# Kernel tuning notes

Hardware: AMD Instinct MI355X
Metric: run time of the kernel (lower is better)

The kernel has to match this reference:

```python
import jax, jax.numpy as jnp
import numpy as np

EPS = 1e-8  # torch cosine_similarity eps


def setup_inputs() -> dict:
    key = jax.random.key(0)
    ks = jax.random.split(key, 8)
    B, D = 65536, 1024
    s = lambda fi, fo: (1.0 / np.sqrt(fi))
    return {
        "image_features": jax.random.normal(ks[0], (B, D), jnp.float32),
        "W1": jax.random.normal(ks[1], (D, 512), jnp.float32) * s(D, 512),
        "b1": jnp.zeros((512,), jnp.float32),
        "W2": jax.random.normal(ks[2], (512, 256), jnp.float32) * s(512, 256),
        "b2": jnp.zeros((256,), jnp.float32),
        "W3": jax.random.normal(ks[3], (256, 128), jnp.float32) * s(256, 128),
        "b3": jnp.zeros((128,), jnp.float32),
        "emb": jax.random.normal(ks[4], (1000, 128), jnp.float32),
    }


def reference(image_features, W1, b1, W2, b2, W3, b3, emb):
    # MLP projection (dropout is identity at inference)
    h = jax.nn.relu(image_features @ W1 + b1)
    h = jax.nn.relu(h @ W2 + b2)
    proj = h @ W3 + b3                              # [B, 128]
    # cosine similarity against all 1000 scene embeddings, fused as
    # normalize + small matmul instead of the broadcasted [B,1000,128] tensor
    pn = proj / jnp.maximum(jnp.linalg.norm(proj, axis=-1, keepdims=True), EPS)
    en = emb / jnp.maximum(jnp.linalg.norm(emb, axis=-1, keepdims=True), EPS)
    sims = pn @ en.T                                # [B, 1000]
    top_indices = jnp.argmax(sims, axis=1)          # [B]
    return top_indices
```

## Files before the change

kernel.cpp:

```cpp
#include <hip/hip_runtime.h>
#include <math.h>

#define EPS 1e-8f
#define TAU 1e-4f

typedef _Float16 half_t;
typedef __attribute__((ext_vector_type(8))) _Float16 f16x8;
typedef __attribute__((ext_vector_type(4))) float f32x4;

__device__ __forceinline__ void gload16(const half_t* g, half_t* l) {
    __builtin_amdgcn_global_load_lds((const __attribute__((address_space(1))) void*)g,
                                     (__attribute__((address_space(3))) void*)l, 16, 0, 0);
}

__device__ __forceinline__ void split2(float a, half_t& h, half_t& l) {
    h = (half_t)a;
    l = (half_t)(a - (float)h);
}


__global__ __launch_bounds__(64) void emb_norm_kernel(const float* __restrict__ emb,
                                                      float* __restrict__ enT) {
    const int row = blockIdx.x;
    const int t = threadIdx.x;
    float e0 = emb[row * 128 + t];
    float e1 = emb[row * 128 + 64 + t];
    float s = e0 * e0 + e1 * e1;
#pragma unroll
    for (int off = 32; off >= 1; off >>= 1) s += __shfl_xor(s, off);
    float denom = fmaxf(sqrtf(s), EPS);
    enT[(size_t)t * 1000 + row]        = e0 / denom;
    enT[(size_t)(64 + t) * 1000 + row] = e1 / denom;
}

__global__ __launch_bounds__(64) void emb_split_kernel(const float* __restrict__ emb,
                                                       half_t* __restrict__ eTh,
                                                       half_t* __restrict__ eTl) {
    const int n = blockIdx.x;
    const int t = threadIdx.x;
    float e0 = 0.f, e1 = 0.f;
    if (n < 1000) {
        e0 = emb[n * 128 + t];
        e1 = emb[n * 128 + 64 + t];
    }
    float s = e0 * e0 + e1 * e1;
#pragma unroll
    for (int off = 32; off >= 1; off >>= 1) s += __shfl_xor(s, off);
    float denom = fmaxf(sqrtf(s), EPS);
    float v0 = (n < 1000) ? e0 / denom : 0.f;
    float v1 = (n < 1000) ? e1 / denom : 0.f;
    half_t h, l;
    int f0 = t, f1 = 64 + t;
    size_t p0 = ((size_t)(f0 >> 3) * 1024 + n) * 8 + (f0 & 7);
    size_t p1 = ((size_t)(f1 >> 3) * 1024 + n) * 8 + (f1 & 7);
    split2(v0, h, l); eTh[p0] = h; eTl[p0] = l;
    split2(v1, h, l); eTh[p1] = h; eTl[p1] = l;
}

template<int N>
__global__ __launch_bounds__(256) void wsplit_kernel(const float* __restrict__ W,
                                                     half_t* __restrict__ Wh,
                                                     half_t* __restrict__ Wl) {
    int idx = blockIdx.x * 256 + threadIdx.x;
    int k = idx / N, n = idx % N;
    float w = W[idx];
    half_t h, l;
    split2(w, h, l);
    size_t pos = ((size_t)(k >> 3) * N + n) * 8 + (k & 7);
    Wh[pos] = h; Wl[pos] = l;
}

#define EPI_RELU 0
#define EPI_NORM 1
#define EPI_TOP2 2

template<int K, int N, bool AF32, int EPI>
__global__ __launch_bounds__(256, 2) void gemm16(
    const float* __restrict__ A32,
    const half_t* __restrict__ Agh, const half_t* __restrict__ Agl,
    const half_t* __restrict__ Bgh, const half_t* __restrict__ Bgl,
    const float* __restrict__ bias,
    half_t* __restrict__ Oh, half_t* __restrict__ Ol,
    float* __restrict__ pv1, int* __restrict__ pi1, float* __restrict__ pv2,
    int Mtot)
{
    __shared__ alignas(16) half_t sAh[8][128][8];
    __shared__ alignas(16) half_t sAl[8][128][8];
    __shared__ alignas(16) half_t sBh[8][128][8];
    __shared__ alignas(16) half_t sBl[8][128][8];

    const int t = threadIdx.x;
    const int lane = t & 63, w = t >> 6;
    const int lr = lane & 15, lg = lane >> 4;
    const int wm = w >> 1, wn = w & 1;

    const int nwg = gridDim.x * gridDim.y;
    const int lin = blockIdx.x + gridDim.x * blockIdx.y;
    const int cpx = nwg >> 3;
    const int logical = (lin & 7) * cpx + (lin >> 3);
    const int bx = logical % gridDim.x;
    const int by = logical / gridDim.x;
    const int m0 = by * 128, n0 = bx * 128;

    f32x4 acc[4][4] = {};

    for (int k0 = 0; k0 < K; k0 += 64) {
        if constexpr (AF32) {
#pragma unroll
            for (int q = 0; q < 4; ++q) {
                int s = t + 256 * q;
                int row = s >> 3, kb = s & 7;
                const float* src = A32 + (size_t)(m0 + row) * K + k0 + kb * 8;
                float4 v0 = *(const float4*)src;
                float4 v1 = *(const float4*)(src + 4);
                float vv[8] = {v0.x, v0.y, v0.z, v0.w, v1.x, v1.y, v1.z, v1.w};
                f16x8 hi, lo;
#pragma unroll
                for (int i = 0; i < 8; ++i) {
                    half_t h = (half_t)vv[i];
                    hi[i] = h;
                    lo[i] = (half_t)(vv[i] - (float)h);
                }
                int prow = row ^ kb;
                *(f16x8*)&sAh[kb][prow][0] = hi;
                *(f16x8*)&sAl[kb][prow][0] = lo;
            }
        } else {
#pragma unroll
            for (int i = 0; i < 4; ++i) {
                int s = (w << 8) + (i << 6) + lane;
                int kb = s >> 7, prow = s & 127;
                int row = prow ^ kb;
                size_t go = (size_t)(m0 + row) * K + k0 + kb * 8;
                gload16(Agh + go, &sAh[0][0][0] + (size_t)s * 8);
                gload16(Agl + go, &sAl[0][0][0] + (size_t)s * 8);
            }
        }
#pragma unroll
        for (int i = 0; i < 4; ++i) {
            int s = (w << 8) + (i << 6) + lane;
            int kb = s >> 7, col = s & 127;
            size_t go = ((size_t)(k0 / 8 + kb) * N + n0 + col) * 8;
            gload16(Bgh + go, &sBh[0][0][0] + (size_t)s * 8);
            gload16(Bgl + go, &sBl[0][0][0] + (size_t)s * 8);
        }
        __syncthreads();
#pragma unroll
        for (int ks = 0; ks < 2; ++ks) {
            const int kb = ks * 4 + lg;
            f16x8 ah[4], al[4], bh[4], bl[4];
#pragma unroll
            for (int mf = 0; mf < 4; ++mf) {
                int row = wm * 64 + mf * 16 + lr;
                int prow = row ^ kb;
                ah[mf] = *(const f16x8*)&sAh[kb][prow][0];
                al[mf] = *(const f16x8*)&sAl[kb][prow][0];
            }
#pragma unroll
            for (int nf = 0; nf < 4; ++nf) {
                int col = wn * 64 + nf * 16 + lr;
                bh[nf] = *(const f16x8*)&sBh[kb][col][0];
                bl[nf] = *(const f16x8*)&sBl[kb][col][0];
            }
#pragma unroll
            for (int mf = 0; mf < 4; ++mf)
#pragma unroll
                for (int nf = 0; nf < 4; ++nf) {
                    acc[mf][nf] = __builtin_amdgcn_mfma_f32_16x16x32_f16(ah[mf], bh[nf], acc[mf][nf], 0, 0, 0);
                    acc[mf][nf] = __builtin_amdgcn_mfma_f32_16x16x32_f16(ah[mf], bl[nf], acc[mf][nf], 0, 0, 0);
                    acc[mf][nf] = __builtin_amdgcn_mfma_f32_16x16x32_f16(al[mf], bh[nf], acc[mf][nf], 0, 0, 0);
                }
        }
        __syncthreads();
    }

    if constexpr (EPI == EPI_RELU) {
#pragma unroll
        for (int nf = 0; nf < 4; ++nf) {
            int n = n0 + wn * 64 + nf * 16 + lr;
            float bb = bias[n];
#pragma unroll
            for (int mf = 0; mf < 4; ++mf)
#pragma unroll
                for (int r = 0; r < 4; ++r) {
                    int m = m0 + wm * 64 + mf * 16 + lg * 4 + r;
                    float v = acc[mf][nf][r] + bb;
                    v = fmaxf(v, 0.f);
                    half_t h, l;
                    split2(v, h, l);
                    Oh[(size_t)m * N + n] = h;
                    Ol[(size_t)m * N + n] = l;
                }
        }
    } else if constexpr (EPI == EPI_NORM) {
        __shared__ float nsum[2][128];
#pragma unroll
        for (int nf = 0; nf < 4; ++nf) {
            float bb = bias[wn * 64 + nf * 16 + lr];
#pragma unroll
            for (int mf = 0; mf < 4; ++mf)
#pragma unroll
                for (int r = 0; r < 4; ++r) acc[mf][nf][r] += bb;
        }
#pragma unroll
        for (int mf = 0; mf < 4; ++mf)
#pragma unroll
            for (int r = 0; r < 4; ++r) {
                float s = 0.f;
#pragma unroll
                for (int nf = 0; nf < 4; ++nf) {
                    float v = acc[mf][nf][r];
                    s += v * v;
                }
#pragma unroll
                for (int off = 1; off < 16; off <<= 1) s += __shfl_xor(s, off);
                if (lr == 0) nsum[wn][wm * 64 + mf * 16 + lg * 4 + r] = s;
            }
        __syncthreads();
#pragma unroll
        for (int mf = 0; mf < 4; ++mf)
#pragma unroll
            for (int r = 0; r < 4; ++r) {
                int ml = wm * 64 + mf * 16 + lg * 4 + r;
                float tot = nsum[0][ml] + nsum[1][ml];
                float sc = 1.0f / fmaxf(sqrtf(tot), EPS);
                int m = m0 + ml;
#pragma unroll
                for (int nf = 0; nf < 4; ++nf) {
                    int n = wn * 64 + nf * 16 + lr;
                    float v = acc[mf][nf][r] * sc;
                    half_t h, l;
                    split2(v, h, l);
                    Oh[(size_t)m * 128 + n] = h;
                    Ol[(size_t)m * 128 + n] = l;
                }
            }
    } else {
        __shared__ float sv1[2][128];
        __shared__ int   si1[2][128];
        __shared__ float sv2[2][128];
#pragma unroll
        for (int mf = 0; mf < 4; ++mf)
#pragma unroll
            for (int r = 0; r < 4; ++r) {
                float v1 = -INFINITY, v2 = -INFINITY;
                int i1 = 0;
#pragma unroll
                for (int nf = 0; nf < 4; ++nf) {
                    int n = n0 + wn * 64 + nf * 16 + lr;
                    float v = (n < 1000) ? acc[mf][nf][r] : -INFINITY;
                    if (v > v1) { v2 = v1; v1 = v; i1 = n; }
                    else if (v > v2) v2 = v;
                }
#pragma unroll
                for (int off = 1; off < 16; off <<= 1) {
                    float ov1 = __shfl_xor(v1, off);
                    int   oi1 = __shfl_xor(i1, off);
                    float ov2 = __shfl_xor(v2, off);
                    if (ov1 > v1) { v2 = fmaxf(v1, ov2); v1 = ov1; i1 = oi1; }
                    else if (ov1 == v1) { v2 = fmaxf(v2, ov1); if (oi1 < i1) i1 = oi1; }
                    else { v2 = fmaxf(v2, ov1); }
                }
                if (lr == 0) {
                    int ml = wm * 64 + mf * 16 + lg * 4 + r;
                    sv1[wn][ml] = v1; si1[wn][ml] = i1; sv2[wn][ml] = v2;
                }
            }
        __syncthreads();
        if (t < 128) {
            float v1 = sv1[0][t]; int i1 = si1[0][t]; float v2 = sv2[0][t];
            float ov1 = sv1[1][t]; int oi1 = si1[1][t]; float ov2 = sv2[1][t];
            if (ov1 > v1) { v2 = fmaxf(v1, ov2); v1 = ov1; i1 = oi1; }
            else if (ov1 == v1) { v2 = fmaxf(v2, ov1); if (oi1 < i1) i1 = oi1; }
            else { v2 = fmaxf(v2, ov1); }
            size_t p = (size_t)bx * Mtot + m0 + t;
            pv1[p] = v1; pi1[p] = i1; pv2[p] = v2;
        }
    }
}

__global__ __launch_bounds__(256) void finalize_kernel(
    const float* __restrict__ pv1, const int* __restrict__ pi1, const float* __restrict__ pv2,
    int* __restrict__ out, int* __restrict__ list, int* __restrict__ count, int Mtot)
{
    int r = blockIdx.x * 256 + threadIdx.x;
    float v1 = -INFINITY, v2 = -INFINITY;
    int i1 = 0;
#pragma unroll
    for (int nb = 0; nb < 8; ++nb) {
        size_t p = (size_t)nb * Mtot + r;
        float ov1 = pv1[p]; int oi1 = pi1[p]; float ov2 = pv2[p];
        if (ov1 > v1) { v2 = fmaxf(v1, ov2); v1 = ov1; i1 = oi1; }
        else if (ov1 == v1) { v2 = fmaxf(v2, ov1); if (oi1 < i1) i1 = oi1; }
        else { v2 = fmaxf(v2, ov1); }
    }
    out[r] = i1;
    if (v1 - v2 < TAU) {
        int p = atomicAdd(count, 1);
        if (p < Mtot) list[p] = r;
    }
}

__global__ void zero_count_kernel(int* c) { if (threadIdx.x == 0) *c = 0; }

__global__ __launch_bounds__(256) void recheck_row_kernel(
    const float* __restrict__ img,
    const float* __restrict__ W1, const float* __restrict__ b1,
    const float* __restrict__ W2, const float* __restrict__ b2,
    const float* __restrict__ W3, const float* __restrict__ b3,
    const float* __restrict__ enT,
    const int* __restrict__ list, const int* __restrict__ count,
    int* __restrict__ out, int maxcnt)
{
    __shared__ float sx[1024];
    __shared__ float sh1[512];
    __shared__ float sh2[256];
    __shared__ float sp[128];
    __shared__ float sden;
    __shared__ float redv[4];
    __shared__ int   redi[4];

    const int t = threadIdx.x;
    const int lane = t & 63, wv = t >> 6;
    int cnt = *count;
    if (cnt > maxcnt) cnt = maxcnt;

    for (int b = blockIdx.x; b < cnt; b += gridDim.x) {
        const int row = list[b];
        *(float4*)&sx[t * 4] = *(const float4*)(img + (size_t)row * 1024 + t * 4);
        __syncthreads();
        {
            float a0 = 0.f, a1 = 0.f;
#pragma unroll 8
            for (int k = 0; k < 1024; ++k) {
                float xv = sx[k];
                float2 wv2 = *(const float2*)(W1 + (size_t)k * 512 + 2 * t);
                a0 = fmaf(xv, wv2.x, a0);
                a1 = fmaf(xv, wv2.y, a1);
            }
            sh1[2 * t]     = fmaxf(a0 + b1[2 * t], 0.f);
            sh1[2 * t + 1] = fmaxf(a1 + b1[2 * t + 1], 0.f);
        }
        __syncthreads();
        {
            float a = 0.f;
#pragma unroll 8
            for (int k = 0; k < 512; ++k)
                a = fmaf(sh1[k], W2[(size_t)k * 256 + t], a);
            sh2[t] = fmaxf(a + b2[t], 0.f);
        }
        __syncthreads();
        if (t < 128) {
            float a = 0.f;
#pragma unroll 8
            for (int k = 0; k < 256; ++k)
                a = fmaf(sh2[k], W3[(size_t)k * 128 + t], a);
            sp[t] = a + b3[t];
        }
        __syncthreads();
        if (t < 64) {
            float s = sp[t] * sp[t] + sp[t + 64] * sp[t + 64];
#pragma unroll
            for (int off = 32; off >= 1; off >>= 1) s += __shfl_xor(s, off);
            if (t == 0) sden = fmaxf(sqrtf(s), EPS);
        }
        __syncthreads();
        if (t < 128) sp[t] = sp[t] / sden;
        __syncthreads();
        float bm = -INFINITY;
        int bi = 0;
#pragma unroll
        for (int j = 0; j < 4; ++j) {
            const int c = t + 256 * j;
            if (c < 1000) {
                float a = 0.f;
#pragma unroll 8
                for (int k = 0; k < 128; ++k)
                    a = fmaf(sp[k], enT[(size_t)k * 1000 + c], a);
                if (a > bm) { bm = a; bi = c; }
            }
        }
#pragma unroll
        for (int off = 1; off < 64; off <<= 1) {
            float om = __shfl_xor(bm, off);
            int oi = __shfl_xor(bi, off);
            if (om > bm || (om == bm && oi < bi)) { bm = om; bi = oi; }
        }
        if (lane == 0) { redv[wv] = bm; redi[wv] = bi; }
        __syncthreads();
        if (t == 0) {
            float v = redv[0]; int i = redi[0];
#pragma unroll
            for (int q = 1; q < 4; ++q) {
                if (redv[q] > v || (redv[q] == v && redi[q] < i)) { v = redv[q]; i = redi[q]; }
            }
            out[row] = i;
        }
        __syncthreads();
    }
}

__global__ __launch_bounds__(256) void scene_exact_kernel(
    const float* __restrict__ img,
    const float* __restrict__ W1, const float* __restrict__ b1,
    const float* __restrict__ W2, const float* __restrict__ b2,
    const float* __restrict__ W3, const float* __restrict__ b3,
    const float* __restrict__ enT,
    int* __restrict__ out)
{
    __shared__ float sImg[16][64];
    __shared__ float sH1[16][512];
    __shared__ float sH2[16][256];
    __shared__ float sPn[16][128];

    const int tid = threadIdx.x;
    const int base = blockIdx.x * 16;

    {
        const int tx = tid & 63, ty = tid >> 6;
        float acc[4][8] = {};
        for (int k0 = 0; k0 < 1024; k0 += 64) {
            {
                const int r = tid >> 4, c4 = tid & 15;
                float4 v = *(const float4*)(img + (size_t)(base + r) * 1024 + k0 + c4 * 4);
                *(float4*)(&sImg[r][c4 * 4]) = v;
            }
            __syncthreads();
#pragma unroll 4
            for (int kk = 0; kk < 64; ++kk) {
                const int k = k0 + kk;
                float a[4];
#pragma unroll
                for (int i = 0; i < 4; ++i) a[i] = sImg[ty + 4 * i][kk];
#pragma unroll
                for (int j = 0; j < 8; ++j) {
                    float wv = W1[(size_t)k * 512 + tx + 64 * j];
#pragma unroll
                    for (int i = 0; i < 4; ++i) acc[i][j] = fmaf(a[i], wv, acc[i][j]);
                }
            }
            __syncthreads();
        }
#pragma unroll
        for (int j = 0; j < 8; ++j) {
            float bb = b1[tx + 64 * j];
#pragma unroll
            for (int i = 0; i < 4; ++i) {
                float v = acc[i][j] + bb;
                sH1[ty + 4 * i][tx + 64 * j] = v > 0.f ? v : 0.f;
            }
        }
        __syncthreads();
    }
    {
        const int tx = tid & 63, ty = tid >> 6;
        float acc[4][4] = {};
#pragma unroll 4
        for (int k = 0; k < 512; ++k) {
            float a[4];
#pragma unroll
            for (int i = 0; i < 4; ++i) a[i] = sH1[ty + 4 * i][k];
#pragma unroll
            for (int j = 0; j < 4; ++j) {
                float wv = W2[(size_t)k * 256 + tx + 64 * j];
#pragma unroll
                for (int i = 0; i < 4; ++i) acc[i][j] = fmaf(a[i], wv, acc[i][j]);
            }
        }
        __syncthreads();
#pragma unroll
        for (int j = 0; j < 4; ++j) {
            float bb = b2[tx + 64 * j];
#pragma unroll
            for (int i = 0; i < 4; ++i) {
                float v = acc[i][j] + bb;
                sH2[ty + 4 * i][tx + 64 * j] = v > 0.f ? v : 0.f;
            }
        }
        __syncthreads();
    }
    {
        const int tx = tid & 31, ty = tid >> 5;
        float acc[2][4] = {};
#pragma unroll 4
        for (int k = 0; k < 256; ++k) {
            float a[2];
#pragma unroll
            for (int i = 0; i < 2; ++i) a[i] = sH2[ty + 8 * i][k];
#pragma unroll
            for (int j = 0; j < 4; ++j) {
                float wv = W3[(size_t)k * 128 + tx + 32 * j];
#pragma unroll
                for (int i = 0; i < 2; ++i) acc[i][j] = fmaf(a[i], wv, acc[i][j]);
            }
        }
#pragma unroll
        for (int j = 0; j < 4; ++j) {
            float bb = b3[tx + 32 * j];
#pragma unroll
            for (int i = 0; i < 2; ++i) sPn[ty + 8 * i][tx + 32 * j] = acc[i][j] + bb;
        }
        __syncthreads();
    }
    {
        const int r = tid >> 4, sub = tid & 15;
        float s = 0.f;
#pragma unroll
        for (int m = 0; m < 8; ++m) {
            float v = sPn[r][sub + 16 * m];
            s += v * v;
        }
#pragma unroll
        for (int off = 1; off < 16; off <<= 1) s += __shfl_xor(s, off);
        float denom = fmaxf(sqrtf(s), EPS);
#pragma unroll
        for (int m = 0; m < 8; ++m) sPn[r][sub + 16 * m] /= denom;
        __syncthreads();
    }
    {
        const int ct = tid & 63, rg = tid >> 6;
        float bm[4]; int bi[4];
#pragma unroll
        for (int i = 0; i < 4; ++i) { bm[i] = -INFINITY; bi[i] = 0; }
#pragma unroll
        for (int tpass = 0; tpass < 2; ++tpass) {
            const int tt = ct + 64 * tpass;
            if (tt < 125) {
                const int c0 = tt * 8;
                float acc[4][8] = {};
#pragma unroll 4
                for (int k = 0; k < 128; ++k) {
                    float p[4];
#pragma unroll
                    for (int i = 0; i < 4; ++i) p[i] = sPn[rg * 4 + i][k];
                    const float* ep = enT + (size_t)k * 1000 + c0;
                    float4 e0 = *(const float4*)(ep);
                    float4 e1 = *(const float4*)(ep + 4);
                    float e[8] = {e0.x, e0.y, e0.z, e0.w, e1.x, e1.y, e1.z, e1.w};
#pragma unroll
                    for (int j = 0; j < 8; ++j)
#pragma unroll
                        for (int i = 0; i < 4; ++i) acc[i][j] = fmaf(p[i], e[j], acc[i][j]);
                }
#pragma unroll
                for (int j = 0; j < 8; ++j) {
                    const int c = c0 + j;
#pragma unroll
                    for (int i = 0; i < 4; ++i)
                        if (acc[i][j] > bm[i]) { bm[i] = acc[i][j]; bi[i] = c; }
                }
            }
        }
#pragma unroll
        for (int off = 1; off < 64; off <<= 1) {
#pragma unroll
            for (int i = 0; i < 4; ++i) {
                float om = __shfl_xor(bm[i], off);
                int oi = __shfl_xor(bi[i], off);
                if (om > bm[i] || (om == bm[i] && oi < bi[i])) { bm[i] = om; bi[i] = oi; }
            }
        }
        if (ct == 0) {
#pragma unroll
            for (int i = 0; i < 4; ++i) out[base + rg * 4 + i] = bi[i];
        }
    }
}

extern "C" void kernel_launch(void* const* d_in, const int* in_sizes, int n_in,
                              void* d_out, int out_size, void* d_ws, size_t ws_size,
                              hipStream_t stream) {
    const float* img = (const float*)d_in[0];
    const float* W1  = (const float*)d_in[1];
    const float* b1  = (const float*)d_in[2];
    const float* W2  = (const float*)d_in[3];
    const float* b2  = (const float*)d_in[4];
    const float* W3  = (const float*)d_in[5];
    const float* b3  = (const float*)d_in[6];
    const float* emb = (const float*)d_in[7];
    int* out = (int*)d_out;
    const int B = in_sizes[0] / 1024;

    size_t off = 0;
    auto carve = [&](size_t bytes) {
        void* p = (char*)d_ws + off;
        off += (bytes + 255) & ~(size_t)255;
        return p;
    };
    float*  enT  = (float*)carve(128 * 1000 * 4);
    half_t* W1h  = (half_t*)carve((size_t)1024 * 512 * 2);
    half_t* W1l  = (half_t*)carve((size_t)1024 * 512 * 2);
    half_t* W2h  = (half_t*)carve((size_t)512 * 256 * 2);
    half_t* W2l  = (half_t*)carve((size_t)512 * 256 * 2);
    half_t* W3h  = (half_t*)carve((size_t)256 * 128 * 2);
    half_t* W3l  = (half_t*)carve((size_t)256 * 128 * 2);
    half_t* eTh  = (half_t*)carve((size_t)16 * 1024 * 8 * 2);
    half_t* eTl  = (half_t*)carve((size_t)16 * 1024 * 8 * 2);
    half_t* h1h  = (half_t*)carve((size_t)B * 512 * 2);
    half_t* h1l  = (half_t*)carve((size_t)B * 512 * 2);
    half_t* h2h  = (half_t*)carve((size_t)B * 256 * 2);
    half_t* h2l  = (half_t*)carve((size_t)B * 256 * 2);
    const size_t REQUIRE = off;

    if (ws_size < REQUIRE) {
        emb_norm_kernel<<<1000, 64, 0, stream>>>(emb, (float*)d_ws);
        scene_exact_kernel<<<B / 16, 256, 0, stream>>>(
            img, W1, b1, W2, b2, W3, b3, (float*)d_ws, out);
        return;
    }

    half_t* pnh  = h1h;
    half_t* pnl  = (half_t*)((char*)h1h + (size_t)B * 128 * 2);
    float*  pv1  = (float*)((char*)h1h + (size_t)B * 128 * 4);
    int*    pi1  = (int*)((char*)pv1 + (size_t)8 * B * 4);
    float*  pv2  = (float*)((char*)pi1 + (size_t)8 * B * 4);
    int*    list = (int*)((char*)pv2 + (size_t)8 * B * 4);
    int*    cnt  = (int*)((char*)list + (size_t)B * 4);

    emb_norm_kernel<<<1000, 64, 0, stream>>>(emb, enT);
    emb_split_kernel<<<1024, 64, 0, stream>>>(emb, eTh, eTl);
    wsplit_kernel<512><<<(1024 * 512) / 256, 256, 0, stream>>>(W1, W1h, W1l);
    wsplit_kernel<256><<<(512 * 256) / 256, 256, 0, stream>>>(W2, W2h, W2l);
    wsplit_kernel<128><<<(256 * 128) / 256, 256, 0, stream>>>(W3, W3h, W3l);

    gemm16<1024, 512, true, EPI_RELU><<<dim3(4, B / 128), 256, 0, stream>>>(
        img, nullptr, nullptr, W1h, W1l, b1, h1h, h1l, nullptr, nullptr, nullptr, B);
    gemm16<512, 256, false, EPI_RELU><<<dim3(2, B / 128), 256, 0, stream>>>(
        nullptr, h1h, h1l, W2h, W2l, b2, h2h, h2l, nullptr, nullptr, nullptr, B);
    gemm16<256, 128, false, EPI_NORM><<<dim3(1, B / 128), 256, 0, stream>>>(
        nullptr, h2h, h2l, W3h, W3l, b3, pnh, pnl, nullptr, nullptr, nullptr, B);
    gemm16<128, 1024, false, EPI_TOP2><<<dim3(8, B / 128), 256, 0, stream>>>(
        nullptr, pnh, pnl, eTh, eTl, nullptr, nullptr, nullptr, pv1, pi1, pv2, B);

    zero_count_kernel<<<1, 64, 0, stream>>>(cnt);
    finalize_kernel<<<B / 256, 256, 0, stream>>>(pv1, pi1, pv2, out, list, cnt, B);
    recheck_row_kernel<<<2048, 256, 0, stream>>>(
        img, W1, b1, W2, b2, W3, b3, enT, list, cnt, out, B);
}
```

Baseline: 621.9 us.

## Fuse third GEMM, normalization, similarity GEMM and top-2 into one kernel

Replaces the separate layer-3 GEMM with norm epilogue, the similarity GEMM with per-tile top-2 partials, and the finalize kernel with one proj_sims kernel. Each 128-row block computes the projection, normalizes it into LDS, loops over the eight 128-column embedding tiles while keeping a running top-2 in registers, and writes the argmax and recheck list directly. This drops the global round trips for the normalized projection and the partial top-2 arrays, plus two launches. In exchange it uses 128 KB of LDS per block with one block per CU, and the embedding tiles are loaded without double buffering.

```diff
diff --git a/kernel.cpp b/kernel.cpp
--- a/kernel.cpp
+++ b/kernel.cpp
@@ -70,19 +70,13 @@
     Wh[pos] = h; Wl[pos] = l;
 }
 
-#define EPI_RELU 0
-#define EPI_NORM 1
-#define EPI_TOP2 2
-
-template<int K, int N, bool AF32, int EPI>
+template<int K, int N, bool AF32>
 __global__ __launch_bounds__(256, 2) void gemm16(
     const float* __restrict__ A32,
     const half_t* __restrict__ Agh, const half_t* __restrict__ Agl,
     const half_t* __restrict__ Bgh, const half_t* __restrict__ Bgl,
     const float* __restrict__ bias,
-    half_t* __restrict__ Oh, half_t* __restrict__ Ol,
-    float* __restrict__ pv1, int* __restrict__ pi1, float* __restrict__ pv2,
-    int Mtot)
+    half_t* __restrict__ Oh, half_t* __restrict__ Ol)
 {
     __shared__ alignas(16) half_t sAh[8][128][8];
     __shared__ alignas(16) half_t sAl[8][128][8];
@@ -174,134 +168,234 @@
         __syncthreads();
     }
 
-    if constexpr (EPI == EPI_RELU) {
-#pragma unroll
-        for (int nf = 0; nf < 4; ++nf) {
-            int n = n0 + wn * 64 + nf * 16 + lr;
-            float bb = bias[n];
+#pragma unroll
+    for (int nf = 0; nf < 4; ++nf) {
+        int n = n0 + wn * 64 + nf * 16 + lr;
+        float bb = bias[n];
+#pragma unroll
+        for (int mf = 0; mf < 4; ++mf)
+#pragma unroll
+            for (int r = 0; r < 4; ++r) {
+                int m = m0 + wm * 64 + mf * 16 + lg * 4 + r;
+                float v = acc[mf][nf][r] + bb;
+                v = fmaxf(v, 0.f);
+                half_t h, l;
+                split2(v, h, l);
+                Oh[(size_t)m * N + n] = h;
+                Ol[(size_t)m * N + n] = l;
+            }
+    }
+}
+
+__global__ void zero_count_kernel(int* c) { if (threadIdx.x == 0) *c = 0; }
+
+__global__ __launch_bounds__(256, 1) void proj_sims_kernel(
+    const half_t* __restrict__ h2h, const half_t* __restrict__ h2l,
+    const half_t* __restrict__ W3h, const half_t* __restrict__ W3l,
+    const float* __restrict__ b3,
+    const half_t* __restrict__ eTh, const half_t* __restrict__ eTl,
+    int* __restrict__ out, int* __restrict__ list, int* __restrict__ cnt,
+    int Mtot)
+{
+    __shared__ alignas(16) unsigned char smem[131072];
+    half_t* sAh = (half_t*)smem;
+    half_t* sAl = sAh + 8 * 128 * 8;
+    half_t* sBh = sAl + 8 * 128 * 8;
+    half_t* sBl = sBh + 8 * 128 * 8;
+    half_t* sPnH = (half_t*)(smem + 65536);
+    half_t* sPnL = sPnH + 16 * 128 * 8;
+    half_t* eH = (half_t*)smem;
+    half_t* eL = eH + 16 * 128 * 8;
+    float* nsum = (float*)smem;
+    float* sv1 = (float*)smem;
+    int*   si1 = (int*)(smem + 1024);
+    float* sv2 = (float*)(smem + 2048);
+
+    const int t = threadIdx.x;
+    const int lane = t & 63, w = t >> 6;
+    const int lr = lane & 15, lg = lane >> 4;
+    const int wm = w >> 1, wn = w & 1;
+    const int m0 = blockIdx.x * 128;
+
+    f32x4 acc[4][4] = {};
+    for (int k0 = 0; k0 < 256; k0 += 64) {
+#pragma unroll
+        for (int i = 0; i < 4; ++i) {
+            int s = (w << 8) + (i << 6) + lane;
+            int kb = s >> 7, prow = s & 127;
+            int row = prow ^ kb;
+            size_t go = (size_t)(m0 + row) * 256 + k0 + kb * 8;
+            gload16(h2h + go, sAh + (size_t)s * 8);
+            gload16(h2l + go, sAl + (size_t)s * 8);
+            int col = s & 127;
+            size_t gb = ((size_t)(k0 / 8 + kb) * 128 + col) * 8;
+            gload16(W3h + gb, sBh + (size_t)s * 8);
+            gload16(W3l + gb, sBl + (size_t)s * 8);
+        }
+        __syncthreads();
+#pragma unroll
+        for (int ks = 0; ks < 2; ++ks) {
+            const int kb = ks * 4 + lg;
+            f16x8 ah[4], al[4], bh[4], bl[4];
+#pragma unroll
+            for (int mf = 0; mf < 4; ++mf) {
+                int prow = (wm * 64 + mf * 16 + lr) ^ kb;
+                ah[mf] = *(const f16x8*)(sAh + ((size_t)kb * 128 + prow) * 8);
+                al[mf] = *(const f16x8*)(sAl + ((size_t)kb * 128 + prow) * 8);
+            }
+#pragma unroll
+            for (int nf = 0; nf < 4; ++nf) {
+                int col = wn * 64 + nf * 16 + lr;
+                bh[nf] = *(const f16x8*)(sBh + ((size_t)kb * 128 + col) * 8);
+                bl[nf] = *(const f16x8*)(sBl + ((size_t)kb * 128 + col) * 8);
+            }
 #pragma unroll
             for (int mf = 0; mf < 4; ++mf)
 #pragma unroll
+                for (int nf = 0; nf < 4; ++nf) {
+                    acc[mf][nf] = __builtin_amdgcn_mfma_f32_16x16x32_f16(ah[mf], bh[nf], acc[mf][nf], 0, 0, 0);
+                    acc[mf][nf] = __builtin_amdgcn_mfma_f32_16x16x32_f16(ah[mf], bl[nf], acc[mf][nf], 0, 0, 0);
+                    acc[mf][nf] = __builtin_amdgcn_mfma_f32_16x16x32_f16(al[mf], bh[nf], acc[mf][nf], 0, 0, 0);
+                }
+        }
+        __syncthreads();
+    }
+
+#pragma unroll
+    for (int nf = 0; nf < 4; ++nf) {
+        float bb = b3[wn * 64 + nf * 16 + lr];
+#pragma unroll
+        for (int mf = 0; mf < 4; ++mf)
+#pragma unroll
+            for (int r = 0; r < 4; ++r) acc[mf][nf][r] += bb;
+    }
+#pragma unroll
+    for (int mf = 0; mf < 4; ++mf)
+#pragma unroll
+        for (int r = 0; r < 4; ++r) {
+            float s = 0.f;
+#pragma unroll
+            for (int nf = 0; nf < 4; ++nf) {
+                float v = acc[mf][nf][r];
+                s += v * v;
+            }
+#pragma unroll
+            for (int off = 1; off < 16; off <<= 1) s += __shfl_xor(s, off);
+            if (lr == 0) nsum[wn * 128 + wm * 64 + mf * 16 + lg * 4 + r] = s;
+        }
+    __syncthreads();
+#pragma unroll
+    for (int mf = 0; mf < 4; ++mf)
+#pragma unroll
+        for (int r = 0; r < 4; ++r) {
+            int row = wm * 64 + mf * 16 + lg * 4 + r;
+            float tot = nsum[row] + nsum[128 + row];
+            float sc = 1.0f / fmaxf(sqrtf(tot), EPS);
+#pragma unroll
+            for (int nf = 0; nf < 4; ++nf) {
+                int col = wn * 64 + nf * 16 + lr;
+                int kb = col >> 3, i = col & 7;
+                int prow = row ^ kb;
+                half_t h, l;
+                split2(acc[mf][nf][r] * sc, h, l);
+                sPnH[((size_t)kb * 128 + prow) * 8 + i] = h;
+                sPnL[((size_t)kb * 128 + prow) * 8 + i] = l;
+            }
+        }
+    __syncthreads();
+
+    float tv1[4][4], tv2[4][4];
+    int ti1[4][4];
+#pragma unroll
+    for (int mf = 0; mf < 4; ++mf)
+#pragma unroll
+        for (int r = 0; r < 4; ++r) { tv1[mf][r] = -INFINITY; tv2[mf][r] = -INFINITY; ti1[mf][r] = 0; }
+
+    for (int nt = 0; nt < 8; ++nt) {
+#pragma unroll
+        for (int i = 0; i < 8; ++i) {
+            int s = t + 256 * i;
+            int kb = s >> 7, col = s & 127;
+            size_t go = ((size_t)kb * 1024 + nt * 128 + col) * 8;
+            gload16(eTh + go, eH + (size_t)s * 8);
+            gload16(eTl + go, eL + (size_t)s * 8);
+        }
+        __syncthreads();
+        f32x4 acc2[4][4] = {};
+#pragma unroll
+        for (int ks = 0; ks < 4; ++ks) {
+            const int kb = ks * 4 + lg;
+            f16x8 ah[4], al[4], bh[4], bl[4];
+#pragma unroll
+            for (int mf = 0; mf < 4; ++mf) {
+                int prow = (wm * 64 + mf * 16 + lr) ^ kb;
+                ah[mf] = *(const f16x8*)(sPnH + ((size_t)kb * 128 + prow) * 8);
+                al[mf] = *(const f16x8*)(sPnL + ((size_t)kb * 128 + prow) * 8);
+            }
+#pragma unroll
+            for (int nf = 0; nf < 4; ++nf) {
+                int col = wn * 64 + nf * 16 + lr;
+                bh[nf] = *(const f16x8*)(eH + ((size_t)kb * 128 + col) * 8);
+                bl[nf] = *(const f16x8*)(eL + ((size_t)kb * 128 + col) * 8);
+            }
+#pragma unroll
+            for (int mf = 0; mf < 4; ++mf)
+#pragma unroll
+                for (int nf = 0; nf < 4; ++nf) {
+                    acc2[mf][nf] = __builtin_amdgcn_mfma_f32_16x16x32_f16(ah[mf], bh[nf], acc2[mf][nf], 0, 0, 0);
+                    acc2[mf][nf] = __builtin_amdgcn_mfma_f32_16x16x32_f16(ah[mf], bl[nf], acc2[mf][nf], 0, 0, 0);
+                    acc2[mf][nf] = __builtin_amdgcn_mfma_f32_16x16x32_f16(al[mf], bh[nf], acc2[mf][nf], 0, 0, 0);
+                }
+        }
+#pragma unroll
+        for (int mf = 0; mf < 4; ++mf)
+#pragma unroll
+            for (int nf = 0; nf < 4; ++nf) {
+                int gc = nt * 128 + wn * 64 + nf * 16 + lr;
+#pragma unroll
                 for (int r = 0; r < 4; ++r) {
-                    int m = m0 + wm * 64 + mf * 16 + lg * 4 + r;
-                    float v = acc[mf][nf][r] + bb;
-                    v = fmaxf(v, 0.f);
-                    half_t h, l;
-                    split2(v, h, l);
-                    Oh[(size_t)m * N + n] = h;
-                    Ol[(size_t)m * N + n] = l;
+                    float v = (gc < 1000) ? acc2[mf][nf][r] : -INFINITY;
+                    if (v > tv1[mf][r]) { tv2[mf][r] = tv1[mf][r]; tv1[mf][r] = v; ti1[mf][r] = gc; }
+                    else if (v > tv2[mf][r]) tv2[mf][r] = v;
                 }
-        }
-    } else if constexpr (EPI == EPI_NORM) {
-        __shared__ float nsum[2][128];
-#pragma unroll
-        for (int nf = 0; nf < 4; ++nf) {
-            float bb = bias[wn * 64 + nf * 16 + lr];
-#pragma unroll
-            for (int mf = 0; mf < 4; ++mf)
-#pragma unroll
-                for (int r = 0; r < 4; ++r) acc[mf][nf][r] += bb;
-        }
-#pragma unroll
-        for (int mf = 0; mf < 4; ++mf)
-#pragma unroll
-            for (int r = 0; r < 4; ++r) {
-                float s = 0.f;
-#pragma unroll
-                for (int nf = 0; nf < 4; ++nf) {
-                    float v = acc[mf][nf][r];
-                    s += v * v;
-                }
-#pragma unroll
-                for (int off = 1; off < 16; off <<= 1) s += __shfl_xor(s, off);
-                if (lr == 0) nsum[wn][wm * 64 + mf * 16 + lg * 4 + r] = s;
-            }
-        __syncthreads();
-#pragma unroll
-        for (int mf = 0; mf < 4; ++mf)
-#pragma unroll
-            for (int r = 0; r < 4; ++r) {
+            }
+        __syncthreads();
+    }
+
+#pragma unroll
+    for (int mf = 0; mf < 4; ++mf)
+#pragma unroll
+        for (int r = 0; r < 4; ++r) {
+            float v1 = tv1[mf][r], v2 = tv2[mf][r];
+            int i1 = ti1[mf][r];
+#pragma unroll
+            for (int off = 1; off < 16; off <<= 1) {
+                float ov1 = __shfl_xor(v1, off);
+                int   oi1 = __shfl_xor(i1, off);
+                float ov2 = __shfl_xor(v2, off);
+                if (ov1 > v1) { v2 = fmaxf(v1, ov2); v1 = ov1; i1 = oi1; }
+                else if (ov1 == v1) { v2 = fmaxf(v2, ov1); if (oi1 < i1) i1 = oi1; }
+                else { v2 = fmaxf(v2, ov1); }
+            }
+            if (lr == 0) {
                 int ml = wm * 64 + mf * 16 + lg * 4 + r;
-                float tot = nsum[0][ml] + nsum[1][ml];
-                float sc = 1.0f / fmaxf(sqrtf(tot), EPS);
-                int m = m0 + ml;
-#pragma unroll
-                for (int nf = 0; nf < 4; ++nf) {
-                    int n = wn * 64 + nf * 16 + lr;
-                    float v = acc[mf][nf][r] * sc;
-                    half_t h, l;
-                    split2(v, h, l);
-                    Oh[(size_t)m * 128 + n] = h;
-                    Ol[(size_t)m * 128 + n] = l;
-                }
-            }
-    } else {
-        __shared__ float sv1[2][128];
-        __shared__ int   si1[2][128];
-        __shared__ float sv2[2][128];
-#pragma unroll
-        for (int mf = 0; mf < 4; ++mf)
-#pragma unroll
-            for (int r = 0; r < 4; ++r) {
-                float v1 = -INFINITY, v2 = -INFINITY;
-                int i1 = 0;
-#pragma unroll
-                for (int nf = 0; nf < 4; ++nf) {
-                    int n = n0 + wn * 64 + nf * 16 + lr;
-                    float v = (n < 1000) ? acc[mf][nf][r] : -INFINITY;
-                    if (v > v1) { v2 = v1; v1 = v; i1 = n; }
-                    else if (v > v2) v2 = v;
-                }
-#pragma unroll
-                for (int off = 1; off < 16; off <<= 1) {
-                    float ov1 = __shfl_xor(v1, off);
-                    int   oi1 = __shfl_xor(i1, off);
-                    float ov2 = __shfl_xor(v2, off);
-                    if (ov1 > v1) { v2 = fmaxf(v1, ov2); v1 = ov1; i1 = oi1; }
-                    else if (ov1 == v1) { v2 = fmaxf(v2, ov1); if (oi1 < i1) i1 = oi1; }
-                    else { v2 = fmaxf(v2, ov1); }
-                }
-                if (lr == 0) {
-                    int ml = wm * 64 + mf * 16 + lg * 4 + r;
-                    sv1[wn][ml] = v1; si1[wn][ml] = i1; sv2[wn][ml] = v2;
-                }
-            }
-        __syncthreads();
-        if (t < 128) {
-            float v1 = sv1[0][t]; int i1 = si1[0][t]; float v2 = sv2[0][t];
-            float ov1 = sv1[1][t]; int oi1 = si1[1][t]; float ov2 = sv2[1][t];
-            if (ov1 > v1) { v2 = fmaxf(v1, ov2); v1 = ov1; i1 = oi1; }
-            else if (ov1 == v1) { v2 = fmaxf(v2, ov1); if (oi1 < i1) i1 = oi1; }
-            else { v2 = fmaxf(v2, ov1); }
-            size_t p = (size_t)bx * Mtot + m0 + t;
-            pv1[p] = v1; pi1[p] = i1; pv2[p] = v2;
-        }
-    }
-}
-
-__global__ __launch_bounds__(256) void finalize_kernel(
-    const float* __restrict__ pv1, const int* __restrict__ pi1, const float* __restrict__ pv2,
-    int* __restrict__ out, int* __restrict__ list, int* __restrict__ count, int Mtot)
-{
-    int r = blockIdx.x * 256 + threadIdx.x;
-    float v1 = -INFINITY, v2 = -INFINITY;
-    int i1 = 0;
-#pragma unroll
-    for (int nb = 0; nb < 8; ++nb) {
-        size_t p = (size_t)nb * Mtot + r;
-        float ov1 = pv1[p]; int oi1 = pi1[p]; float ov2 = pv2[p];
+                sv1[wn * 128 + ml] = v1; si1[wn * 128 + ml] = i1; sv2[wn * 128 + ml] = v2;
+            }
+        }
+    __syncthreads();
+    if (t < 128) {
+        float v1 = sv1[t]; int i1 = si1[t]; float v2 = sv2[t];
+        float ov1 = sv1[128 + t]; int oi1 = si1[128 + t]; float ov2 = sv2[128 + t];
         if (ov1 > v1) { v2 = fmaxf(v1, ov2); v1 = ov1; i1 = oi1; }
         else if (ov1 == v1) { v2 = fmaxf(v2, ov1); if (oi1 < i1) i1 = oi1; }
         else { v2 = fmaxf(v2, ov1); }
-    }
-    out[r] = i1;
-    if (v1 - v2 < TAU) {
-        int p = atomicAdd(count, 1);
-        if (p < Mtot) list[p] = r;
-    }
-}
-
-__global__ void zero_count_kernel(int* c) { if (threadIdx.x == 0) *c = 0; }
+        out[m0 + t] = i1;
+        if (v1 - v2 < TAU) {
+            int p = atomicAdd(cnt, 1);
+            if (p < Mtot) list[p] = m0 + t;
+        }
+    }
+}
 
 __global__ __launch_bounds__(256) void recheck_row_kernel(
     const float* __restrict__ img,
@@ -609,13 +703,8 @@
         return;
     }
 
-    half_t* pnh  = h1h;
-    half_t* pnl  = (half_t*)((char*)h1h + (size_t)B * 128 * 2);
-    float*  pv1  = (float*)((char*)h1h + (size_t)B * 128 * 4);
-    int*    pi1  = (int*)((char*)pv1 + (size_t)8 * B * 4);
-    float*  pv2  = (float*)((char*)pi1 + (size_t)8 * B * 4);
-    int*    list = (int*)((char*)pv2 + (size_t)8 * B * 4);
-    int*    cnt  = (int*)((char*)list + (size_t)B * 4);
+    int* list = (int*)h1h;
+    int* cnt  = (int*)((char*)h1h + (size_t)B * 4);
 
     emb_norm_kernel<<<1000, 64, 0, stream>>>(emb, enT);
     emb_split_kernel<<<1024, 64, 0, stream>>>(emb, eTh, eTl);
@@ -623,17 +712,15 @@
     wsplit_kernel<256><<<(512 * 256) / 256, 256, 0, stream>>>(W2, W2h, W2l);
     wsplit_kernel<128><<<(256 * 128) / 256, 256, 0, stream>>>(W3, W3h, W3l);
 
-    gemm16<1024, 512, true, EPI_RELU><<<dim3(4, B / 128), 256, 0, stream>>>(
-        img, nullptr, nullptr, W1h, W1l, b1, h1h, h1l, nullptr, nullptr, nullptr, B);
-    gemm16<512, 256, false, EPI_RELU><<<dim3(2, B / 128), 256, 0, stream>>>(
-        nullptr, h1h, h1l, W2h, W2l, b2, h2h, h2l, nullptr, nullptr, nullptr, B);
-    gemm16<256, 128, false, EPI_NORM><<<dim3(1, B / 128), 256, 0, stream>>>(
-        nullptr, h2h, h2l, W3h, W3l, b3, pnh, pnl, nullptr, nullptr, nullptr, B);
-    gemm16<128, 1024, false, EPI_TOP2><<<dim3(8, B / 128), 256, 0, stream>>>(
-        nullptr, pnh, pnl, eTh, eTl, nullptr, nullptr, nullptr, pv1, pi1, pv2, B);
+    gemm16<1024, 512, true><<<dim3(4, B / 128), 256, 0, stream>>>(
+        img, nullptr, nullptr, W1h, W1l, b1, h1h, h1l);
+    gemm16<512, 256, false><<<dim3(2, B / 128), 256, 0, stream>>>(
+        nullptr, h1h, h1l, W2h, W2l, b2, h2h, h2l);
 
     zero_count_kernel<<<1, 64, 0, stream>>>(cnt);
-    finalize_kernel<<<B / 256, 256, 0, stream>>>(pv1, pi1, pv2, out, list, cnt, B);
+    proj_sims_kernel<<<B / 128, 256, 0, stream>>>(
+        h2h, h2l, W3h, W3l, b3, eTh, eTl, out, list, cnt, B);
+
     recheck_row_kernel<<<2048, 256, 0, stream>>>(
         img, W1, b1, W2, b2, W3, b3, enT, list, cnt, out, B);
 }
```

Result: slower. 1.133 ms (+82.2%).

## Fuse similarity GEMM, top-2 reduction and finalize into one row-tiled kernel

Applied to the files above, without the earlier changes.

Replaces the 128x128-tiled similarity GEMM with per-N-tile partial top-2 outputs plus a separate finalize kernel by a single kernel. Each block keeps a 64-row slice of normalized projections resident in LDS and streams all 16 embedding column tiles, holding a running top-2 in registers. The block then writes the argmax and ambiguous-row list directly. This removes the partial-result buffers, their global round trip and one launch. In exchange, embedding tiles are reloaded per 64-row block and loads are not double-buffered, so each tile waits on its load.

```diff
diff --git a/kernel.cpp b/kernel.cpp
--- a/kernel.cpp
+++ b/kernel.cpp
@@ -72,7 +72,6 @@
 
 #define EPI_RELU 0
 #define EPI_NORM 1
-#define EPI_TOP2 2
 
 template<int K, int N, bool AF32, int EPI>
 __global__ __launch_bounds__(256, 2) void gemm16(
@@ -80,9 +79,7 @@
     const half_t* __restrict__ Agh, const half_t* __restrict__ Agl,
     const half_t* __restrict__ Bgh, const half_t* __restrict__ Bgl,
     const float* __restrict__ bias,
-    half_t* __restrict__ Oh, half_t* __restrict__ Ol,
-    float* __restrict__ pv1, int* __restrict__ pi1, float* __restrict__ pv2,
-    int Mtot)
+    half_t* __restrict__ Oh, half_t* __restrict__ Ol)
 {
     __shared__ alignas(16) half_t sAh[8][128][8];
     __shared__ alignas(16) half_t sAl[8][128][8];
@@ -192,7 +189,7 @@
                     Ol[(size_t)m * N + n] = l;
                 }
         }
-    } else if constexpr (EPI == EPI_NORM) {
+    } else {
         __shared__ float nsum[2][128];
 #pragma unroll
         for (int nf = 0; nf < 4; ++nf) {
@@ -235,73 +232,143 @@
                     Ol[(size_t)m * 128 + n] = l;
                 }
             }
-    } else {
-        __shared__ float sv1[2][128];
-        __shared__ int   si1[2][128];
-        __shared__ float sv2[2][128];
-#pragma unroll
-        for (int mf = 0; mf < 4; ++mf)
-#pragma unroll
-            for (int r = 0; r < 4; ++r) {
-                float v1 = -INFINITY, v2 = -INFINITY;
-                int i1 = 0;
-#pragma unroll
-                for (int nf = 0; nf < 4; ++nf) {
-                    int n = n0 + wn * 64 + nf * 16 + lr;
-                    float v = (n < 1000) ? acc[mf][nf][r] : -INFINITY;
-                    if (v > v1) { v2 = v1; v1 = v; i1 = n; }
-                    else if (v > v2) v2 = v;
-                }
-#pragma unroll
-                for (int off = 1; off < 16; off <<= 1) {
-                    float ov1 = __shfl_xor(v1, off);
-                    int   oi1 = __shfl_xor(i1, off);
-                    float ov2 = __shfl_xor(v2, off);
-                    if (ov1 > v1) { v2 = fmaxf(v1, ov2); v1 = ov1; i1 = oi1; }
-                    else if (ov1 == v1) { v2 = fmaxf(v2, ov1); if (oi1 < i1) i1 = oi1; }
-                    else { v2 = fmaxf(v2, ov1); }
-                }
-                if (lr == 0) {
-                    int ml = wm * 64 + mf * 16 + lg * 4 + r;
-                    sv1[wn][ml] = v1; si1[wn][ml] = i1; sv2[wn][ml] = v2;
-                }
-            }
-        __syncthreads();
-        if (t < 128) {
-            float v1 = sv1[0][t]; int i1 = si1[0][t]; float v2 = sv2[0][t];
-            float ov1 = sv1[1][t]; int oi1 = si1[1][t]; float ov2 = sv2[1][t];
-            if (ov1 > v1) { v2 = fmaxf(v1, ov2); v1 = ov1; i1 = oi1; }
-            else if (ov1 == v1) { v2 = fmaxf(v2, ov1); if (oi1 < i1) i1 = oi1; }
-            else { v2 = fmaxf(v2, ov1); }
-            size_t p = (size_t)bx * Mtot + m0 + t;
-            pv1[p] = v1; pi1[p] = i1; pv2[p] = v2;
-        }
-    }
-}
-
-__global__ __launch_bounds__(256) void finalize_kernel(
-    const float* __restrict__ pv1, const int* __restrict__ pi1, const float* __restrict__ pv2,
-    int* __restrict__ out, int* __restrict__ list, int* __restrict__ count, int Mtot)
+    }
+}
+
+__global__ void zero_count_kernel(int* c) { if (threadIdx.x == 0) *c = 0; }
+
+__global__ __launch_bounds__(256, 2) void sims64_kernel(
+    const half_t* __restrict__ pnh, const half_t* __restrict__ pnl,
+    const half_t* __restrict__ eTh, const half_t* __restrict__ eTl,
+    int* __restrict__ out, int* __restrict__ list, int* __restrict__ cnt,
+    int Mtot)
 {
-    int r = blockIdx.x * 256 + threadIdx.x;
-    float v1 = -INFINITY, v2 = -INFINITY;
-    int i1 = 0;
-#pragma unroll
-    for (int nb = 0; nb < 8; ++nb) {
-        size_t p = (size_t)nb * Mtot + r;
-        float ov1 = pv1[p]; int oi1 = pi1[p]; float ov2 = pv2[p];
+    __shared__ alignas(16) half_t sPnH[16 * 64 * 8];
+    __shared__ alignas(16) half_t sPnL[16 * 64 * 8];
+    __shared__ alignas(16) half_t sEH[16 * 64 * 8];
+    __shared__ alignas(16) half_t sEL[16 * 64 * 8];
+    __shared__ float sv1[128];
+    __shared__ int   si1[128];
+    __shared__ float sv2[128];
+
+    const int t = threadIdx.x;
+    const int lane = t & 63, w = t >> 6;
+    const int lr = lane & 15, lg = lane >> 4;
+    const int wm = w >> 1, wn = w & 1;
+    const int m0 = blockIdx.x * 64;
+
+#pragma unroll
+    for (int i = 0; i < 4; ++i) {
+        int s = t + 256 * i;
+        int kb = s >> 6, row = s & 63;
+        size_t go = (size_t)(m0 + row) * 128 + kb * 8;
+        gload16(pnh + go, sPnH + (size_t)s * 8);
+        gload16(pnl + go, sPnL + (size_t)s * 8);
+    }
+#pragma unroll
+    for (int i = 0; i < 4; ++i) {
+        int s = t + 256 * i;
+        int kb = s >> 6, col = s & 63;
+        size_t go = ((size_t)kb * 1024 + col) * 8;
+        gload16(eTh + go, sEH + (size_t)s * 8);
+        gload16(eTl + go, sEL + (size_t)s * 8);
+    }
+
+    float tv1[2][4], tv2[2][4];
+    int ti1[2][4];
+#pragma unroll
+    for (int mf = 0; mf < 2; ++mf)
+#pragma unroll
+        for (int r = 0; r < 4; ++r) { tv1[mf][r] = -INFINITY; tv2[mf][r] = -INFINITY; ti1[mf][r] = 0; }
+
+    for (int nt = 0; nt < 16; ++nt) {
+        __syncthreads();
+        f32x4 acc[2][2] = {};
+#pragma unroll
+        for (int ks = 0; ks < 4; ++ks) {
+            const int kb = ks * 4 + lg;
+            f16x8 ah[2], al[2], bh[2], bl[2];
+#pragma unroll
+            for (int mf = 0; mf < 2; ++mf) {
+                int row = wm * 32 + mf * 16 + lr;
+                ah[mf] = *(const f16x8*)(sPnH + ((size_t)kb * 64 + row) * 8);
+                al[mf] = *(const f16x8*)(sPnL + ((size_t)kb * 64 + row) * 8);
+            }
+#pragma unroll
+            for (int nf = 0; nf < 2; ++nf) {
+                int col = wn * 32 + nf * 16 + lr;
+                bh[nf] = *(const f16x8*)(sEH + ((size_t)kb * 64 + col) * 8);
+                bl[nf] = *(const f16x8*)(sEL + ((size_t)kb * 64 + col) * 8);
+            }
+#pragma unroll
+            for (int mf = 0; mf < 2; ++mf)
+#pragma unroll
+                for (int nf = 0; nf < 2; ++nf) {
+                    acc[mf][nf] = __builtin_amdgcn_mfma_f32_16x16x32_f16(ah[mf], bh[nf], acc[mf][nf], 0, 0, 0);
+                    acc[mf][nf] = __builtin_amdgcn_mfma_f32_16x16x32_f16(ah[mf], bl[nf], acc[mf][nf], 0, 0, 0);
+                    acc[mf][nf] = __builtin_amdgcn_mfma_f32_16x16x32_f16(al[mf], bh[nf], acc[mf][nf], 0, 0, 0);
+                }
+        }
+#pragma unroll
+        for (int mf = 0; mf < 2; ++mf)
+#pragma unroll
+            for (int nf = 0; nf < 2; ++nf) {
+                int gc = nt * 64 + wn * 32 + nf * 16 + lr;
+#pragma unroll
+                for (int r = 0; r < 4; ++r) {
+                    float v = (gc < 1000) ? acc[mf][nf][r] : -INFINITY;
+                    if (v > tv1[mf][r]) { tv2[mf][r] = tv1[mf][r]; tv1[mf][r] = v; ti1[mf][r] = gc; }
+                    else if (v > tv2[mf][r]) tv2[mf][r] = v;
+                }
+            }
+        __syncthreads();
+        if (nt < 15) {
+            int ntn = nt + 1;
+#pragma unroll
+            for (int i = 0; i < 4; ++i) {
+                int s = t + 256 * i;
+                int kb = s >> 6, col = s & 63;
+                size_t go = ((size_t)kb * 1024 + ntn * 64 + col) * 8;
+                gload16(eTh + go, sEH + (size_t)s * 8);
+                gload16(eTl + go, sEL + (size_t)s * 8);
+            }
+        }
+    }
+
+#pragma unroll
+    for (int mf = 0; mf < 2; ++mf)
+#pragma unroll
+        for (int r = 0; r < 4; ++r) {
+            float v1 = tv1[mf][r], v2 = tv2[mf][r];
+            int i1 = ti1[mf][r];
+#pragma unroll
+            for (int off = 1; off < 16; off <<= 1) {
+                float ov1 = __shfl_xor(v1, off);
+                int   oi1 = __shfl_xor(i1, off);
+                float ov2 = __shfl_xor(v2, off);
+                if (ov1 > v1) { v2 = fmaxf(v1, ov2); v1 = ov1; i1 = oi1; }
+                else if (ov1 == v1) { v2 = fmaxf(v2, ov1); if (oi1 < i1) i1 = oi1; }
+                else { v2 = fmaxf(v2, ov1); }
+            }
+            if (lr == 0) {
+                int ml = wm * 32 + mf * 16 + lg * 4 + r;
+                sv1[wn * 64 + ml] = v1; si1[wn * 64 + ml] = i1; sv2[wn * 64 + ml] = v2;
+            }
+        }
+    __syncthreads();
+    if (t < 64) {
+        float v1 = sv1[t]; int i1 = si1[t]; float v2 = sv2[t];
+        float ov1 = sv1[64 + t]; int oi1 = si1[64 + t]; float ov2 = sv2[64 + t];
         if (ov1 > v1) { v2 = fmaxf(v1, ov2); v1 = ov1; i1 = oi1; }
         else if (ov1 == v1) { v2 = fmaxf(v2, ov1); if (oi1 < i1) i1 = oi1; }
         else { v2 = fmaxf(v2, ov1); }
-    }
-    out[r] = i1;
-    if (v1 - v2 < TAU) {
-        int p = atomicAdd(count, 1);
-        if (p < Mtot) list[p] = r;
-    }
-}
-
-__global__ void zero_count_kernel(int* c) { if (threadIdx.x == 0) *c = 0; }
+        out[m0 + t] = i1;
+        if (v1 - v2 < TAU) {
+            int p = atomicAdd(cnt, 1);
+            if (p < Mtot) list[p] = m0 + t;
+        }
+    }
+}
 
 __global__ __launch_bounds__(256) void recheck_row_kernel(
     const float* __restrict__ img,
@@ -611,10 +678,7 @@
 
     half_t* pnh  = h1h;
     half_t* pnl  = (half_t*)((char*)h1h + (size_t)B * 128 * 2);
-    float*  pv1  = (float*)((char*)h1h + (size_t)B * 128 * 4);
-    int*    pi1  = (int*)((char*)pv1 + (size_t)8 * B * 4);
-    float*  pv2  = (float*)((char*)pi1 + (size_t)8 * B * 4);
-    int*    list = (int*)((char*)pv2 + (size_t)8 * B * 4);
+    int*    list = (int*)((char*)h1h + (size_t)B * 128 * 4);
     int*    cnt  = (int*)((char*)list + (size_t)B * 4);
 
     emb_norm_kernel<<<1000, 64, 0, stream>>>(emb, enT);
@@ -624,16 +688,16 @@
     wsplit_kernel<128><<<(256 * 128) / 256, 256, 0, stream>>>(W3, W3h, W3l);
 
     gemm16<1024, 512, true, EPI_RELU><<<dim3(4, B / 128), 256, 0, stream>>>(
-        img, nullptr, nullptr, W1h, W1l, b1, h1h, h1l, nullptr, nullptr, nullptr, B);
+        img, nullptr, nullptr, W1h, W1l, b1, h1h, h1l);
     gemm16<512, 256, false, EPI_RELU><<<dim3(2, B / 128), 256, 0, stream>>>(
-        nullptr, h1h, h1l, W2h, W2l, b2, h2h, h2l, nullptr, nullptr, nullptr, B);
+        nullptr, h1h, h1l, W2h, W2l, b2, h2h, h2l);
     gemm16<256, 128, false, EPI_NORM><<<dim3(1, B / 128), 256, 0, stream>>>(
-        nullptr, h2h, h2l, W3h, W3l, b3, pnh, pnl, nullptr, nullptr, nullptr, B);
-    gemm16<128, 1024, false, EPI_TOP2><<<dim3(8, B / 128), 256, 0, stream>>>(
-        nullptr, pnh, pnl, eTh, eTl, nullptr, nullptr, nullptr, pv1, pi1, pv2, B);
+        nullptr, h2h, h2l, W3h, W3l, b3, pnh, pnl);
 
     zero_count_kernel<<<1, 64, 0, stream>>>(cnt);
-    finalize_kernel<<<B / 256, 256, 0, stream>>>(pv1, pi1, pv2, out, list, cnt, B);
+    sims64_kernel<<<B / 64, 256, 0, stream>>>(
+        pnh, pnl, eTh, eTl, out, list, cnt, B);
+
     recheck_row_kernel<<<2048, 256, 0, stream>>>(
         img, W1, b1, W2, b2, W3, b3, enT, list, cnt, out, B);
 }
```

Result: faster. 568.6 us (-8.6%).
